# Performance work log

Measured on AMD Instinct MI355X. Metric: run time of the kernel, lower is better.

Reference implementation:

```python
import jax, jax.numpy as jnp
import numpy as np

N_NODES = 50000
N_EDGES = 800000
IN_CH = 128
OUT_CH = 64
H1, C1 = 8, 8            # conv1: heads=8, out=8, concat -> 64
H2, C2 = 1, OUT_CH       # conv2: heads=1, out=64, concat=False
NEG_SLOPE = 0.2


def gat_conv(x, src, dst, W, att_src, att_dst, bias, heads, ch, concat):
    """PyG GATConv (self loops assumed already appended to src/dst).
    x: [N, F_in], W: [F_in, heads*ch], att_*: [heads, ch], bias: [heads*ch] or [ch]."""
    N = x.shape[0]
    h = (x @ W).reshape(N, heads, ch)                       # [N,H,C]
    a_s = jnp.einsum('nhc,hc->nh', h, att_src)              # [N,H]
    a_d = jnp.einsum('nhc,hc->nh', h, att_dst)              # [N,H]
    e = jax.nn.leaky_relu(a_s[src] + a_d[dst], NEG_SLOPE)   # [E,H]
    # segment softmax over incoming edges of each destination node
    m = jax.ops.segment_max(e, dst, num_segments=N)         # [N,H]
    ex = jnp.exp(e - m[dst])
    s = jax.ops.segment_sum(ex, dst, num_segments=N)        # [N,H]
    alpha = ex / (s[dst] + 1e-16)                           # [E,H]
    out = jax.ops.segment_sum(h[src] * alpha[:, :, None], dst, num_segments=N)  # [N,H,C]
    out = out.reshape(N, heads * ch) if concat else out.mean(axis=1)
    return out + bias


def setup_inputs() -> dict:
    key = jax.random.key(0)
    ks = jax.random.split(key, 12)
    glorot = lambda k, shape: jax.random.normal(k, shape, jnp.float32) * np.sqrt(2.0 / (shape[0] + shape[-1]))
    x = jax.random.normal(ks[0], (N_NODES, IN_CH), jnp.float32)
    edge_index = jax.random.randint(ks[1], (2, N_EDGES), 0, N_NODES, jnp.int64 if jax.config.read('jax_enable_x64') else jnp.int32).astype(jnp.int32)
    W1 = glorot(ks[2], (IN_CH, H1 * C1))
    att_src1 = glorot(ks[3], (H1, C1))
    att_dst1 = glorot(ks[4], (H1, C1))
    b1 = jnp.zeros((H1 * C1,), jnp.float32)
    W2 = glorot(ks[5], (H1 * C1, H2 * C2))
    att_src2 = glorot(ks[6], (H2, C2))
    att_dst2 = glorot(ks[7], (H2, C2))
    b2 = jnp.zeros((C2,), jnp.float32)
    return {"x": x, "edge_index": edge_index, "W1": W1, "att_src1": att_src1,
            "att_dst1": att_dst1, "b1": b1, "W2": W2, "att_src2": att_src2,
            "att_dst2": att_dst2, "b2": b2}


def reference(x, edge_index, W1, att_src1, att_dst1, b1, W2, att_src2, att_dst2, b2):
    N = x.shape[0]
    loops = jnp.arange(N, dtype=edge_index.dtype)
    src = jnp.concatenate([edge_index[0], loops])  # add_self_loops=True (PyG default)
    dst = jnp.concatenate([edge_index[1], loops])
    h = gat_conv(x, src, dst, W1, att_src1, att_dst1, b1, H1, C1, concat=True)
    h = jax.nn.elu(h)
    # F.dropout(training=self.training): identity in eval mode
    out = gat_conv(h, src, dst, W2, att_src2, att_dst2, b2, H2, C2, concat=False)
    return out
```

## Files before the change

### kernel.cpp

```cpp
#include <hip/hip_runtime.h>

#define NN 50000
#define NE 800000
#define NEG_SLOPE 0.2f

__device__ __forceinline__ float lrelu(float v) { return v > 0.f ? v : NEG_SLOPE * v; }
__device__ __forceinline__ float bf2f(unsigned short u) { return __uint_as_float((unsigned)u << 16); }
__device__ __forceinline__ unsigned short f2bf(float f) {
    unsigned u = __float_as_uint(f);
    return (unsigned short)((u + 0x7FFFu + ((u >> 16) & 1u)) >> 16);
}
__device__ __forceinline__ float rlane(float v, int l) {
    return __int_as_float(__builtin_amdgcn_readlane(__float_as_int(v), l));
}

__global__ __launch_bounds__(256) void setup(const float* __restrict__ W1,
                                             const float* __restrict__ W2,
                                             const float* __restrict__ as2,
                                             const float* __restrict__ ad2,
                                             int4* __restrict__ deg4,
                                             int* __restrict__ gcursor,
                                             float* __restrict__ W1S,
                                             float* __restrict__ W2S,
                                             float* __restrict__ w_as2,
                                             float* __restrict__ w_ad2) {
    int gid = blockIdx.x * 256 + threadIdx.x;
    if (gid < 12500) deg4[gid] = make_int4(0, 0, 0, 0);
    if (gid == 0) *gcursor = 0;
    if (gid < 8192) {
        int k = gid >> 6, c = gid & 63;
        W1S[((k >> 2) * 64 + c) * 4 + (k & 3)] = W1[k * 64 + c];
    } else if (gid < 12288) {
        int t = gid - 8192;
        int k = t >> 6, c = t & 63;
        W2S[((k >> 2) * 64 + c) * 4 + (k & 3)] = W2[k * 64 + c];
    }
    if (gid < 64) {
        float s = 0.f;
        for (int c = 0; c < 64; ++c) s += W2[gid * 64 + c] * as2[c];
        w_as2[gid] = s;
    } else if (gid < 128) {
        int k = gid - 64;
        float s = 0.f;
        for (int c = 0; c < 64; ++c) s += W2[k * 64 + c] * ad2[c];
        w_ad2[k] = s;
    }
}

__global__ void hist(const int* __restrict__ ei, int* __restrict__ deg,
                     int* __restrict__ rank) {
    int e = blockIdx.x * blockDim.x + threadIdx.x;
    if (e < NE) rank[e] = atomicAdd(&deg[ei[NE + e]], 1);
}

__global__ __launch_bounds__(256) void scanA(const int* __restrict__ deg,
                                             int* __restrict__ offs,
                                             int* __restrict__ gcursor) {
    __shared__ int tmp[256];
    __shared__ int base;
    int i = blockIdx.x * 256 + threadIdx.x;
    int v = (i < NN) ? deg[i] : 0;
    tmp[threadIdx.x] = v;
    __syncthreads();
    for (int o = 1; o < 256; o <<= 1) {
        int t = (threadIdx.x >= o) ? tmp[threadIdx.x - o] : 0;
        __syncthreads();
        tmp[threadIdx.x] += t;
        __syncthreads();
    }
    if (threadIdx.x == 255) base = atomicAdd(gcursor, tmp[255]);
    __syncthreads();
    if (i < NN) offs[i] = base + tmp[threadIdx.x] - v;
}

__global__ void scatter(const int* __restrict__ ei, const int* __restrict__ rank,
                        const int* __restrict__ offs, int* __restrict__ srclist) {
    int e = blockIdx.x * blockDim.x + threadIdx.x;
    if (e < NE) {
        int d = ei[NE + e];
        srclist[offs[d] + rank[e]] = ei[e];
    }
}

__global__ __launch_bounds__(256) void gemm1(const float* __restrict__ x,
                                             const float* __restrict__ W1S,
                                             const float* __restrict__ att_s,
                                             const float* __restrict__ att_d,
                                             unsigned short* __restrict__ h1b,
                                             float* __restrict__ a_s,
                                             float2* __restrict__ nd1) {
    int lane = threadIdx.x & 63;
    int wv   = __builtin_amdgcn_readfirstlane(threadIdx.x >> 6);
    int n0   = blockIdx.x * 16 + wv * 4;
    const float* __restrict__ xr = x + (size_t)n0 * 128;
    const float4* __restrict__ wp = (const float4*)W1S;
    float4 acc = {0.f, 0.f, 0.f, 0.f};
#pragma unroll 4
    for (int k4 = 0; k4 < 32; ++k4) {
        float4 w = wp[k4 * 64 + lane];
        const float* xk = xr + k4 * 4;
        acc.x += xk[0]   * w.x + xk[1]   * w.y + xk[2]   * w.z + xk[3]   * w.w;
        acc.y += xk[128] * w.x + xk[129] * w.y + xk[130] * w.z + xk[131] * w.w;
        acc.z += xk[256] * w.x + xk[257] * w.y + xk[258] * w.z + xk[259] * w.w;
        acc.w += xk[384] * w.x + xk[385] * w.y + xk[386] * w.z + xk[387] * w.w;
    }
    float as_l = att_s[lane], ad_l = att_d[lane];
    float av[4] = {acc.x, acc.y, acc.z, acc.w};
#pragma unroll
    for (int r = 0; r < 4; ++r) {
        float a = av[r];
        h1b[(size_t)(n0 + r) * 64 + lane] = f2bf(a);
        float ps = a * as_l, pd = a * ad_l;
        ps += __shfl_xor(ps, 1, 64); pd += __shfl_xor(pd, 1, 64);
        ps += __shfl_xor(ps, 2, 64); pd += __shfl_xor(pd, 2, 64);
        ps += __shfl_xor(ps, 4, 64); pd += __shfl_xor(pd, 4, 64);
        if ((lane & 7) == 0) {
            int h = lane >> 3;
            a_s[(n0 + r) * 8 + h] = ps;
            nd1[(n0 + r) * 8 + h] = make_float2(pd, lrelu(ps + pd));
        }
    }
}

__global__ __launch_bounds__(256) void agg1(const int* __restrict__ srclist,
                                            const int* __restrict__ offs,
                                            const int* __restrict__ degv,
                                            const float* __restrict__ a_s,
                                            const float2* __restrict__ nd1,
                                            const unsigned short* __restrict__ h1b,
                                            const float* __restrict__ b1,
                                            const float* __restrict__ w_as2,
                                            const float* __restrict__ w_ad2,
                                            unsigned short* __restrict__ xhb,
                                            float* __restrict__ a_s2,
                                            float2* __restrict__ nd2) {
    int wv   = threadIdx.x >> 6;
    int lane = threadIdx.x & 63;
    int d    = blockIdx.x * 4 + wv;
    int base = offs[d], dg = degv[d];
    int sub  = lane >> 3, hch = lane & 7;
    float2 nd = nd1[d * 8 + hch];
    float acc0 = 0.f, acc1 = 0.f, acc2 = 0.f, acc3 = 0.f;
    float acc4 = 0.f, acc5 = 0.f, acc6 = 0.f, acc7 = 0.f;
    float sm = 0.f;
#pragma unroll 2
    for (int k = sub; k < dg; k += 8) {
        int s = srclist[base + k];
        float ex = __expf(lrelu(a_s[s * 8 + hch] + nd.x) - nd.y);
        uint4 hv = *(const uint4*)&h1b[(size_t)s * 64 + hch * 8];
        acc0 += __uint_as_float(hv.x << 16)          * ex;
        acc1 += __uint_as_float(hv.x & 0xffff0000u)  * ex;
        acc2 += __uint_as_float(hv.y << 16)          * ex;
        acc3 += __uint_as_float(hv.y & 0xffff0000u)  * ex;
        acc4 += __uint_as_float(hv.z << 16)          * ex;
        acc5 += __uint_as_float(hv.z & 0xffff0000u)  * ex;
        acc6 += __uint_as_float(hv.w << 16)          * ex;
        acc7 += __uint_as_float(hv.w & 0xffff0000u)  * ex;
        sm += ex;
    }
    if (sub == 0) {
        uint4 hv = *(const uint4*)&h1b[(size_t)d * 64 + hch * 8];
        acc0 += __uint_as_float(hv.x << 16);
        acc1 += __uint_as_float(hv.x & 0xffff0000u);
        acc2 += __uint_as_float(hv.y << 16);
        acc3 += __uint_as_float(hv.y & 0xffff0000u);
        acc4 += __uint_as_float(hv.z << 16);
        acc5 += __uint_as_float(hv.z & 0xffff0000u);
        acc6 += __uint_as_float(hv.w << 16);
        acc7 += __uint_as_float(hv.w & 0xffff0000u);
        sm += 1.f;
    }
#pragma unroll
    for (int m = 8; m < 64; m <<= 1) {
        acc0 += __shfl_xor(acc0, m, 64); acc1 += __shfl_xor(acc1, m, 64);
        acc2 += __shfl_xor(acc2, m, 64); acc3 += __shfl_xor(acc3, m, 64);
        acc4 += __shfl_xor(acc4, m, 64); acc5 += __shfl_xor(acc5, m, 64);
        acc6 += __shfl_xor(acc6, m, 64); acc7 += __shfl_xor(acc7, m, 64);
        sm   += __shfl_xor(sm, m, 64);
    }
    float inv = 1.f / sm;
    int li = (lane & 7) * 8;
    float4 bl = *(const float4*)&b1[li];
    float4 bh = *(const float4*)&b1[li + 4];
    float4 lo, hi;
    lo.x = acc0 * inv + bl.x; lo.x = lo.x > 0.f ? lo.x : expm1f(lo.x);
    lo.y = acc1 * inv + bl.y; lo.y = lo.y > 0.f ? lo.y : expm1f(lo.y);
    lo.z = acc2 * inv + bl.z; lo.z = lo.z > 0.f ? lo.z : expm1f(lo.z);
    lo.w = acc3 * inv + bl.w; lo.w = lo.w > 0.f ? lo.w : expm1f(lo.w);
    hi.x = acc4 * inv + bh.x; hi.x = hi.x > 0.f ? hi.x : expm1f(hi.x);
    hi.y = acc5 * inv + bh.y; hi.y = hi.y > 0.f ? hi.y : expm1f(hi.y);
    hi.z = acc6 * inv + bh.z; hi.z = hi.z > 0.f ? hi.z : expm1f(hi.z);
    hi.w = acc7 * inv + bh.w; hi.w = hi.w > 0.f ? hi.w : expm1f(hi.w);
    if (lane < 8) {
        uint4 pk;
        pk.x = ((unsigned)f2bf(lo.y) << 16) | f2bf(lo.x);
        pk.y = ((unsigned)f2bf(lo.w) << 16) | f2bf(lo.z);
        pk.z = ((unsigned)f2bf(hi.y) << 16) | f2bf(hi.x);
        pk.w = ((unsigned)f2bf(hi.w) << 16) | f2bf(hi.z);
        *(uint4*)&xhb[(size_t)d * 64 + lane * 8] = pk;
    }
    float4 s0 = *(const float4*)&w_as2[li], s1 = *(const float4*)&w_as2[li + 4];
    float4 d0 = *(const float4*)&w_ad2[li], d1 = *(const float4*)&w_ad2[li + 4];
    float ps = lo.x*s0.x + lo.y*s0.y + lo.z*s0.z + lo.w*s0.w
             + hi.x*s1.x + hi.y*s1.y + hi.z*s1.z + hi.w*s1.w;
    float pd = lo.x*d0.x + lo.y*d0.y + lo.z*d0.z + lo.w*d0.w
             + hi.x*d1.x + hi.y*d1.y + hi.z*d1.z + hi.w*d1.w;
    ps += __shfl_xor(ps, 1, 64); pd += __shfl_xor(pd, 1, 64);
    ps += __shfl_xor(ps, 2, 64); pd += __shfl_xor(pd, 2, 64);
    ps += __shfl_xor(ps, 4, 64); pd += __shfl_xor(pd, 4, 64);
    if (lane == 0) {
        a_s2[d] = ps;
        nd2[d]  = make_float2(pd, lrelu(ps + pd));
    }
}

__global__ __launch_bounds__(256) void agg2(const int* __restrict__ srclist,
                                            const int* __restrict__ offs,
                                            const int* __restrict__ degv,
                                            const float* __restrict__ a_s2,
                                            const float2* __restrict__ nd2,
                                            const unsigned short* __restrict__ xhb,
                                            const float* __restrict__ W2S,
                                            const float* __restrict__ b2,
                                            float* __restrict__ out) {
    int wv   = threadIdx.x >> 6;
    int lane = threadIdx.x & 63;
    int d    = blockIdx.x * 4 + wv;
    int base = offs[d], dg = degv[d];
    int sub  = lane >> 3, hch = lane & 7;
    float2 nd = nd2[d];
    float acc0 = 0.f, acc1 = 0.f, acc2 = 0.f, acc3 = 0.f;
    float acc4 = 0.f, acc5 = 0.f, acc6 = 0.f, acc7 = 0.f;
    float sm = 0.f;
#pragma unroll 2
    for (int k = sub; k < dg; k += 8) {
        int s = srclist[base + k];
        float ex = __expf(lrelu(a_s2[s] + nd.x) - nd.y);
        uint4 hv = *(const uint4*)&xhb[(size_t)s * 64 + hch * 8];
        acc0 += __uint_as_float(hv.x << 16)          * ex;
        acc1 += __uint_as_float(hv.x & 0xffff0000u)  * ex;
        acc2 += __uint_as_float(hv.y << 16)          * ex;
        acc3 += __uint_as_float(hv.y & 0xffff0000u)  * ex;
        acc4 += __uint_as_float(hv.z << 16)          * ex;
        acc5 += __uint_as_float(hv.z & 0xffff0000u)  * ex;
        acc6 += __uint_as_float(hv.w << 16)          * ex;
        acc7 += __uint_as_float(hv.w & 0xffff0000u)  * ex;
        sm += ex;
    }
    if (sub == 0) {
        uint4 hv = *(const uint4*)&xhb[(size_t)d * 64 + hch * 8];
        acc0 += __uint_as_float(hv.x << 16);
        acc1 += __uint_as_float(hv.x & 0xffff0000u);
        acc2 += __uint_as_float(hv.y << 16);
        acc3 += __uint_as_float(hv.y & 0xffff0000u);
        acc4 += __uint_as_float(hv.z << 16);
        acc5 += __uint_as_float(hv.z & 0xffff0000u);
        acc6 += __uint_as_float(hv.w << 16);
        acc7 += __uint_as_float(hv.w & 0xffff0000u);
        sm += 1.f;
    }
#pragma unroll
    for (int m = 8; m < 64; m <<= 1) {
        acc0 += __shfl_xor(acc0, m, 64); acc1 += __shfl_xor(acc1, m, 64);
        acc2 += __shfl_xor(acc2, m, 64); acc3 += __shfl_xor(acc3, m, 64);
        acc4 += __shfl_xor(acc4, m, 64); acc5 += __shfl_xor(acc5, m, 64);
        acc6 += __shfl_xor(acc6, m, 64); acc7 += __shfl_xor(acc7, m, 64);
        sm   += __shfl_xor(sm, m, 64);
    }
    float inv = 1.f / sm;
    float t0 = acc0 * inv, t1 = acc1 * inv, t2 = acc2 * inv, t3 = acc3 * inv;
    float t4 = acc4 * inv, t5 = acc5 * inv, t6 = acc6 * inv, t7 = acc7 * inv;
    const float4* wp = (const float4*)W2S;
    float o = 0.f;
#pragma unroll
    for (int k4 = 0; k4 < 16; ++k4) {
        float4 w = wp[k4 * 64 + lane];
        int j = k4 >> 1;
        if (k4 & 1)
            o += rlane(t4, j) * w.x + rlane(t5, j) * w.y + rlane(t6, j) * w.z + rlane(t7, j) * w.w;
        else
            o += rlane(t0, j) * w.x + rlane(t1, j) * w.y + rlane(t2, j) * w.z + rlane(t3, j) * w.w;
    }
    out[(size_t)d * 64 + lane] = o + b2[lane];
}

extern "C" void kernel_launch(void* const* d_in, const int* in_sizes, int n_in,
                              void* d_out, int out_size, void* d_ws, size_t ws_size,
                              hipStream_t stream) {
    const float* x   = (const float*)d_in[0];
    const int*   ei  = (const int*)d_in[1];
    const float* W1  = (const float*)d_in[2];
    const float* as1 = (const float*)d_in[3];
    const float* ad1 = (const float*)d_in[4];
    const float* b1  = (const float*)d_in[5];
    const float* W2  = (const float*)d_in[6];
    const float* as2 = (const float*)d_in[7];
    const float* ad2 = (const float*)d_in[8];
    const float* b2  = (const float*)d_in[9];
    float* out = (float*)d_out;

    float* ws = (float*)d_ws;
    unsigned short* h1b = (unsigned short*)ws;
    unsigned short* xhb = (unsigned short*)(ws + 1600000);
    float*  a_s1 = ws + 3200000;
    float2* nd1  = (float2*)(ws + 3600000);
    float*  a_s2 = ws + 4400000;
    float2* nd2  = (float2*)(ws + 4450000);
    int* deg     = (int*)(ws + 4550000);
    int* offs    = deg + 50000;
    int* gcursor = offs + 50000;
    int* rank    = gcursor + 64;
    int* srclist = rank + 800000;
    float* W1S   = (float*)(srclist + 800000);
    float* W2S   = W1S + 8192;
    float* w_as2 = W2S + 4096;
    float* w_ad2 = w_as2 + 64;

    setup<<<49, 256, 0, stream>>>(W1, W2, as2, ad2, (int4*)deg, gcursor,
                                  W1S, W2S, w_as2, w_ad2);
    hist<<<3125, 256, 0, stream>>>(ei, deg, rank);
    scanA<<<196, 256, 0, stream>>>(deg, offs, gcursor);
    scatter<<<3125, 256, 0, stream>>>(ei, rank, offs, srclist);

    gemm1<<<3125, 256, 0, stream>>>(x, W1S, as1, ad1, h1b, a_s1, nd1);
    agg1<<<12500, 256, 0, stream>>>(srclist, offs, deg, a_s1, nd1, h1b, b1,
                                    w_as2, w_ad2, xhb, a_s2, nd2);

    agg2<<<12500, 256, 0, stream>>>(srclist, offs, deg, a_s2, nd2, xhb, W2S, b2, out);
}
```

Measured before the change: 169.8 us.

## Merge histogram with first GEMM and software-pipeline gather loads in aggregations

The degree histogram and the layer-1 GEMM are independent, so they now run in one launch: the first half of the blocks do the atomic histogram and the second half do the GEMM. This removes a launch and lets the atomic-bound and compute-bound work overlap. Both aggregation loops now prefetch the next source index two steps ahead and the next feature row one step ahead, replacing the unroll pragma. This hides gather latency at the cost of extra registers.

```diff
diff --git a/kernel.cpp b/kernel.cpp
--- a/kernel.cpp
+++ b/kernel.cpp
@@ -5,7 +5,6 @@
 #define NEG_SLOPE 0.2f
 
 __device__ __forceinline__ float lrelu(float v) { return v > 0.f ? v : NEG_SLOPE * v; }
-__device__ __forceinline__ float bf2f(unsigned short u) { return __uint_as_float((unsigned)u << 16); }
 __device__ __forceinline__ unsigned short f2bf(float f) {
     unsigned u = __float_as_uint(f);
     return (unsigned short)((u + 0x7FFFu + ((u >> 16) & 1u)) >> 16);
@@ -47,51 +46,24 @@
     }
 }
 
-__global__ void hist(const int* __restrict__ ei, int* __restrict__ deg,
-                     int* __restrict__ rank) {
-    int e = blockIdx.x * blockDim.x + threadIdx.x;
-    if (e < NE) rank[e] = atomicAdd(&deg[ei[NE + e]], 1);
-}
-
-__global__ __launch_bounds__(256) void scanA(const int* __restrict__ deg,
-                                             int* __restrict__ offs,
-                                             int* __restrict__ gcursor) {
-    __shared__ int tmp[256];
-    __shared__ int base;
-    int i = blockIdx.x * 256 + threadIdx.x;
-    int v = (i < NN) ? deg[i] : 0;
-    tmp[threadIdx.x] = v;
-    __syncthreads();
-    for (int o = 1; o < 256; o <<= 1) {
-        int t = (threadIdx.x >= o) ? tmp[threadIdx.x - o] : 0;
-        __syncthreads();
-        tmp[threadIdx.x] += t;
-        __syncthreads();
-    }
-    if (threadIdx.x == 255) base = atomicAdd(gcursor, tmp[255]);
-    __syncthreads();
-    if (i < NN) offs[i] = base + tmp[threadIdx.x] - v;
-}
-
-__global__ void scatter(const int* __restrict__ ei, const int* __restrict__ rank,
-                        const int* __restrict__ offs, int* __restrict__ srclist) {
-    int e = blockIdx.x * blockDim.x + threadIdx.x;
-    if (e < NE) {
-        int d = ei[NE + e];
-        srclist[offs[d] + rank[e]] = ei[e];
-    }
-}
-
-__global__ __launch_bounds__(256) void gemm1(const float* __restrict__ x,
-                                             const float* __restrict__ W1S,
-                                             const float* __restrict__ att_s,
-                                             const float* __restrict__ att_d,
-                                             unsigned short* __restrict__ h1b,
-                                             float* __restrict__ a_s,
-                                             float2* __restrict__ nd1) {
+__global__ __launch_bounds__(256) void hist_gemm1(const int* __restrict__ ei,
+                                                  int* __restrict__ deg,
+                                                  int* __restrict__ rank,
+                                                  const float* __restrict__ x,
+                                                  const float* __restrict__ W1S,
+                                                  const float* __restrict__ att_s,
+                                                  const float* __restrict__ att_d,
+                                                  unsigned short* __restrict__ h1b,
+                                                  float* __restrict__ a_s,
+                                                  float2* __restrict__ nd1) {
+    if (blockIdx.x < 3125) {
+        int e = blockIdx.x * 256 + threadIdx.x;
+        if (e < NE) rank[e] = atomicAdd(&deg[ei[NE + e]], 1);
+        return;
+    }
     int lane = threadIdx.x & 63;
     int wv   = __builtin_amdgcn_readfirstlane(threadIdx.x >> 6);
-    int n0   = blockIdx.x * 16 + wv * 4;
+    int n0   = (blockIdx.x - 3125) * 16 + wv * 4;
     const float* __restrict__ xr = x + (size_t)n0 * 128;
     const float4* __restrict__ wp = (const float4*)W1S;
     float4 acc = {0.f, 0.f, 0.f, 0.f};
@@ -119,6 +91,35 @@
             a_s[(n0 + r) * 8 + h] = ps;
             nd1[(n0 + r) * 8 + h] = make_float2(pd, lrelu(ps + pd));
         }
+    }
+}
+
+__global__ __launch_bounds__(256) void scanA(const int* __restrict__ deg,
+                                             int* __restrict__ offs,
+                                             int* __restrict__ gcursor) {
+    __shared__ int tmp[256];
+    __shared__ int base;
+    int i = blockIdx.x * 256 + threadIdx.x;
+    int v = (i < NN) ? deg[i] : 0;
+    tmp[threadIdx.x] = v;
+    __syncthreads();
+    for (int o = 1; o < 256; o <<= 1) {
+        int t = (threadIdx.x >= o) ? tmp[threadIdx.x - o] : 0;
+        __syncthreads();
+        tmp[threadIdx.x] += t;
+        __syncthreads();
+    }
+    if (threadIdx.x == 255) base = atomicAdd(gcursor, tmp[255]);
+    __syncthreads();
+    if (i < NN) offs[i] = base + tmp[threadIdx.x] - v;
+}
+
+__global__ void scatter(const int* __restrict__ ei, const int* __restrict__ rank,
+                        const int* __restrict__ offs, int* __restrict__ srclist) {
+    int e = blockIdx.x * blockDim.x + threadIdx.x;
+    if (e < NE) {
+        int d = ei[NE + e];
+        srclist[offs[d] + rank[e]] = ei[e];
     }
 }
 
@@ -143,20 +144,35 @@
     float acc0 = 0.f, acc1 = 0.f, acc2 = 0.f, acc3 = 0.f;
     float acc4 = 0.f, acc5 = 0.f, acc6 = 0.f, acc7 = 0.f;
     float sm = 0.f;
-#pragma unroll 2
-    for (int k = sub; k < dg; k += 8) {
-        int s = srclist[base + k];
-        float ex = __expf(lrelu(a_s[s * 8 + hch] + nd.x) - nd.y);
-        uint4 hv = *(const uint4*)&h1b[(size_t)s * 64 + hch * 8];
-        acc0 += __uint_as_float(hv.x << 16)          * ex;
-        acc1 += __uint_as_float(hv.x & 0xffff0000u)  * ex;
-        acc2 += __uint_as_float(hv.y << 16)          * ex;
-        acc3 += __uint_as_float(hv.y & 0xffff0000u)  * ex;
-        acc4 += __uint_as_float(hv.z << 16)          * ex;
-        acc5 += __uint_as_float(hv.z & 0xffff0000u)  * ex;
-        acc6 += __uint_as_float(hv.w << 16)          * ex;
-        acc7 += __uint_as_float(hv.w & 0xffff0000u)  * ex;
+    int k = sub;
+    int s0 = 0, s1 = 0;
+    float as0 = 0.f;
+    uint4 hv0 = make_uint4(0, 0, 0, 0);
+    if (k < dg)     s0 = srclist[base + k];
+    if (k + 8 < dg) s1 = srclist[base + k + 8];
+    if (k < dg) {
+        as0 = a_s[s0 * 8 + hch];
+        hv0 = *(const uint4*)&h1b[(size_t)s0 * 64 + hch * 8];
+    }
+    for (; k < dg; k += 8) {
+        int   s2  = (k + 16 < dg) ? srclist[base + k + 16] : 0;
+        float as1 = 0.f;
+        uint4 hv1 = make_uint4(0, 0, 0, 0);
+        if (k + 8 < dg) {
+            as1 = a_s[s1 * 8 + hch];
+            hv1 = *(const uint4*)&h1b[(size_t)s1 * 64 + hch * 8];
+        }
+        float ex = __expf(lrelu(as0 + nd.x) - nd.y);
+        acc0 += __uint_as_float(hv0.x << 16)          * ex;
+        acc1 += __uint_as_float(hv0.x & 0xffff0000u)  * ex;
+        acc2 += __uint_as_float(hv0.y << 16)          * ex;
+        acc3 += __uint_as_float(hv0.y & 0xffff0000u)  * ex;
+        acc4 += __uint_as_float(hv0.z << 16)          * ex;
+        acc5 += __uint_as_float(hv0.z & 0xffff0000u)  * ex;
+        acc6 += __uint_as_float(hv0.w << 16)          * ex;
+        acc7 += __uint_as_float(hv0.w & 0xffff0000u)  * ex;
         sm += ex;
+        s0 = s1; s1 = s2; as0 = as1; hv0 = hv1;
     }
     if (sub == 0) {
         uint4 hv = *(const uint4*)&h1b[(size_t)d * 64 + hch * 8];
@@ -199,12 +215,12 @@
         pk.w = ((unsigned)f2bf(hi.w) << 16) | f2bf(hi.z);
         *(uint4*)&xhb[(size_t)d * 64 + lane * 8] = pk;
     }
-    float4 s0 = *(const float4*)&w_as2[li], s1 = *(const float4*)&w_as2[li + 4];
-    float4 d0 = *(const float4*)&w_ad2[li], d1 = *(const float4*)&w_ad2[li + 4];
-    float ps = lo.x*s0.x + lo.y*s0.y + lo.z*s0.z + lo.w*s0.w
-             + hi.x*s1.x + hi.y*s1.y + hi.z*s1.z + hi.w*s1.w;
-    float pd = lo.x*d0.x + lo.y*d0.y + lo.z*d0.z + lo.w*d0.w
-             + hi.x*d1.x + hi.y*d1.y + hi.z*d1.z + hi.w*d1.w;
+    float4 s0v = *(const float4*)&w_as2[li], s1v = *(const float4*)&w_as2[li + 4];
+    float4 d0v = *(const float4*)&w_ad2[li], d1v = *(const float4*)&w_ad2[li + 4];
+    float ps = lo.x*s0v.x + lo.y*s0v.y + lo.z*s0v.z + lo.w*s0v.w
+             + hi.x*s1v.x + hi.y*s1v.y + hi.z*s1v.z + hi.w*s1v.w;
+    float pd = lo.x*d0v.x + lo.y*d0v.y + lo.z*d0v.z + lo.w*d0v.w
+             + hi.x*d1v.x + hi.y*d1v.y + hi.z*d1v.z + hi.w*d1v.w;
     ps += __shfl_xor(ps, 1, 64); pd += __shfl_xor(pd, 1, 64);
     ps += __shfl_xor(ps, 2, 64); pd += __shfl_xor(pd, 2, 64);
     ps += __shfl_xor(ps, 4, 64); pd += __shfl_xor(pd, 4, 64);
@@ -232,20 +248,35 @@
     float acc0 = 0.f, acc1 = 0.f, acc2 = 0.f, acc3 = 0.f;
     float acc4 = 0.f, acc5 = 0.f, acc6 = 0.f, acc7 = 0.f;
     float sm = 0.f;
-#pragma unroll 2
-    for (int k = sub; k < dg; k += 8) {
-        int s = srclist[base + k];
-        float ex = __expf(lrelu(a_s2[s] + nd.x) - nd.y);
-        uint4 hv = *(const uint4*)&xhb[(size_t)s * 64 + hch * 8];
-        acc0 += __uint_as_float(hv.x << 16)          * ex;
-        acc1 += __uint_as_float(hv.x & 0xffff0000u)  * ex;
-        acc2 += __uint_as_float(hv.y << 16)          * ex;
-        acc3 += __uint_as_float(hv.y & 0xffff0000u)  * ex;
-        acc4 += __uint_as_float(hv.z << 16)          * ex;
-        acc5 += __uint_as_float(hv.z & 0xffff0000u)  * ex;
-        acc6 += __uint_as_float(hv.w << 16)          * ex;
-        acc7 += __uint_as_float(hv.w & 0xffff0000u)  * ex;
+    int k = sub;
+    int s0 = 0, s1 = 0;
+    float as0 = 0.f;
+    uint4 hv0 = make_uint4(0, 0, 0, 0);
+    if (k < dg)     s0 = srclist[base + k];
+    if (k + 8 < dg) s1 = srclist[base + k + 8];
+    if (k < dg) {
+        as0 = a_s2[s0];
+        hv0 = *(const uint4*)&xhb[(size_t)s0 * 64 + hch * 8];
+    }
+    for (; k < dg; k += 8) {
+        int   s2  = (k + 16 < dg) ? srclist[base + k + 16] : 0;
+        float as1 = 0.f;
+        uint4 hv1 = make_uint4(0, 0, 0, 0);
+        if (k + 8 < dg) {
+            as1 = a_s2[s1];
+            hv1 = *(const uint4*)&xhb[(size_t)s1 * 64 + hch * 8];
+        }
+        float ex = __expf(lrelu(as0 + nd.x) - nd.y);
+        acc0 += __uint_as_float(hv0.x << 16)          * ex;
+        acc1 += __uint_as_float(hv0.x & 0xffff0000u)  * ex;
+        acc2 += __uint_as_float(hv0.y << 16)          * ex;
+        acc3 += __uint_as_float(hv0.y & 0xffff0000u)  * ex;
+        acc4 += __uint_as_float(hv0.z << 16)          * ex;
+        acc5 += __uint_as_float(hv0.z & 0xffff0000u)  * ex;
+        acc6 += __uint_as_float(hv0.w << 16)          * ex;
+        acc7 += __uint_as_float(hv0.w & 0xffff0000u)  * ex;
         sm += ex;
+        s0 = s1; s1 = s2; as0 = as1; hv0 = hv1;
     }
     if (sub == 0) {
         uint4 hv = *(const uint4*)&xhb[(size_t)d * 64 + hch * 8];
@@ -318,13 +349,12 @@
 
     setup<<<49, 256, 0, stream>>>(W1, W2, as2, ad2, (int4*)deg, gcursor,
                                   W1S, W2S, w_as2, w_ad2);
-    hist<<<3125, 256, 0, stream>>>(ei, deg, rank);
+    hist_gemm1<<<6250, 256, 0, stream>>>(ei, deg, rank, x, W1S, as1, ad1,
+                                         h1b, a_s1, nd1);
     scanA<<<196, 256, 0, stream>>>(deg, offs, gcursor);
     scatter<<<3125, 256, 0, stream>>>(ei, rank, offs, srclist);
 
-    gemm1<<<3125, 256, 0, stream>>>(x, W1S, as1, ad1, h1b, a_s1, nd1);
     agg1<<<12500, 256, 0, stream>>>(srclist, offs, deg, a_s1, nd1, h1b, b1,
                                     w_as2, w_ad2, xhb, a_s2, nd2);
-
     agg2<<<12500, 256, 0, stream>>>(srclist, offs, deg, a_s2, nd2, xhb, W2S, b2, out);
 }
```

New measurement: 160.4 us. -5.5%, faster.
